# Kernel optimization log

Hardware: AMD Instinct MI355X
Metric: run time of the kernel (lower is better)

## Reference

```python
import jax, jax.numpy as jnp
import numpy as np
import math

B, L, H, E = 16, 1024, 8, 64   # L = nsensor = N (forced by einsum 'bhls,bhlg')
WIN = 1024                      # win_size, last dim of x
G = 64                          # n_group
D_SEL = 1                       # d_sel default


def setup_inputs() -> dict:
    key = jax.random.key(0)
    ks = jax.random.split(key, 7)
    return {
        "queries": jax.random.normal(ks[0], (B, L, H, E), dtype=jnp.float32),
        "keys": jax.random.normal(ks[1], (B, L, H, E), dtype=jnp.float32),
        "values": jax.random.normal(ks[2], (B, L, H, E), dtype=jnp.float32),
        "x": jax.random.normal(ks[3], (B, L, WIN), dtype=jnp.float32),
        "mlp_w": jax.random.normal(ks[4], (H * D_SEL, WIN), dtype=jnp.float32) * 0.02,
        "mlp_b": jax.random.normal(ks[5], (H * D_SEL,), dtype=jnp.float32) * 0.02,
        "sel_W": jax.random.normal(ks[6], (H, G, D_SEL), dtype=jnp.float32),
        "attn_mask": 0,
    }


def _select_attention(x, mlp_w, mlp_b, sel_W, n_heads, d_sel):
    b, n, lwin = x.shape
    xf = x.reshape(b * n, lwin)
    newx = jnp.tanh(xf @ mlp_w.T + mlp_b)                 # [(B*N), H*d_sel]
    # Faithful raw reshape (torch.reshape, no permute): mixes n and h axes.
    newx = newx.reshape(b, n_heads, n, d_sel)             # [B, H, N, d_sel]
    sel = jnp.einsum('bhnd,hgd->bhng', newx, sel_W)       # [B, H, N, G]
    return jax.nn.relu(sel)


def reference(queries, keys, values, x, mlp_w, mlp_b, sel_W, attn_mask):
    b, l, h, e = queries.shape
    scale = 1.0 / math.sqrt(e)
    scores = jnp.einsum('blhe,bshe->bhls', queries, keys)      # [B, H, L, S]
    sel = _select_attention(x, mlp_w, mlp_b, sel_W, h, D_SEL)  # [B, H, L, G]
    scores = jnp.einsum('bhls,bhlg->bhsg', scores, sel)        # [B, H, S, G]
    series = jax.nn.softmax(scale * scores, axis=-1)           # softmax over groups
    # values labeled 'blhs': l=S (value len), s=D (feature). Output V: [B, D, H, G]
    V = jnp.einsum('blhs,bhlg->bshg', values, series)
    return V
```

## Files before the change

kernel.cpp:

```cpp
#include <hip/hip_runtime.h>
#include <math.h>

#define NB 16
#define NL 1024
#define NH 8
#define NE 64
#define NWIN 1024
#define NG 64

#define SCH 128
#define SROW 136

typedef __attribute__((ext_vector_type(8))) short short8;
typedef __attribute__((ext_vector_type(4))) float floatx4;

__device__ __forceinline__ short f2bf(float x) {
    unsigned u = __float_as_uint(x);
    u += 0x7fffu + ((u >> 16) & 1u);
    return (short)(u >> 16);
}
__device__ __forceinline__ float dot4(float4 a, float4 b) {
    return fmaf(a.x, b.x, fmaf(a.y, b.y, fmaf(a.z, b.z, a.w * b.w)));
}

__device__ __forceinline__ void lgkm_barrier() {
    asm volatile("s_waitcnt lgkmcnt(0)" ::: "memory");
    __builtin_amdgcn_s_barrier();
}

__global__ __launch_bounds__(256, 4) void k_sel_q(
    const float* __restrict__ x, const float* __restrict__ mlp_w,
    const float* __restrict__ mlp_b, const float* __restrict__ q,
    float* __restrict__ qp, float* __restrict__ qn)
{
    __shared__ float4 w_lds[8][NWIN / 4];
    __shared__ float t_lds[128];
    __shared__ float redp[4][64], redn[4][64];

    int tid = threadIdx.x;
    int blk = blockIdx.x;
    int ee = blk & 7, bh = blk >> 3;
    int b = bh >> 3, h = bh & 7;
    int w = tid >> 6, lane = tid & 63;
    int sq = lane >> 4, c = lane & 15;

    const float4* w4 = (const float4*)mlp_w;
    float4* wl = (float4*)w_lds;
    #pragma unroll
    for (int i = 0; i < 8; ++i)
        wl[tid + 256 * i] = w4[tid + 256 * i];
    __syncthreads();

    int row_loc = w * 4 + sq;
    int r = b * 1024 + h * 128 + ee * 16 + row_loc;
    const float4* xr = (const float4*)(x + (size_t)r * NWIN);
    float4 a03 = make_float4(0,0,0,0), a47 = make_float4(0,0,0,0);
    #pragma unroll
    for (int i = 0; i < 16; ++i) {
        float4 xv = xr[i * 16 + c];
        a03.x += dot4(xv, w_lds[0][i * 16 + c]);
        a03.y += dot4(xv, w_lds[1][i * 16 + c]);
        a03.z += dot4(xv, w_lds[2][i * 16 + c]);
        a03.w += dot4(xv, w_lds[3][i * 16 + c]);
        a47.x += dot4(xv, w_lds[4][i * 16 + c]);
        a47.y += dot4(xv, w_lds[5][i * 16 + c]);
        a47.z += dot4(xv, w_lds[6][i * 16 + c]);
        a47.w += dot4(xv, w_lds[7][i * 16 + c]);
    }
    #pragma unroll
    for (int off = 1; off < 16; off <<= 1) {
        a03.x += __shfl_xor(a03.x, off, 64);
        a03.y += __shfl_xor(a03.y, off, 64);
        a03.z += __shfl_xor(a03.z, off, 64);
        a03.w += __shfl_xor(a03.w, off, 64);
        a47.x += __shfl_xor(a47.x, off, 64);
        a47.y += __shfl_xor(a47.y, off, 64);
        a47.z += __shfl_xor(a47.z, off, 64);
        a47.w += __shfl_xor(a47.w, off, 64);
    }
    if (c == 0) {
        float4 b03 = *(const float4*)mlp_b;
        float4 b47 = *(const float4*)(mlp_b + 4);
        float4 t03, t47;
        t03.x = tanhf(a03.x + b03.x); t03.y = tanhf(a03.y + b03.y);
        t03.z = tanhf(a03.z + b03.z); t03.w = tanhf(a03.w + b03.w);
        t47.x = tanhf(a47.x + b47.x); t47.y = tanhf(a47.y + b47.y);
        t47.z = tanhf(a47.z + b47.z); t47.w = tanhf(a47.w + b47.w);
        *(float4*)&t_lds[row_loc * 8]     = t03;
        *(float4*)&t_lds[row_loc * 8 + 4] = t47;
    }
    __syncthreads();

    int lo = sq, e4 = c;
    float4 accp = make_float4(0,0,0,0), accn = make_float4(0,0,0,0);
    #pragma unroll
    for (int i = 0; i < 8; ++i) {
        int l_loc = w * 32 + i * 4 + lo;
        float tv = t_lds[l_loc];
        int l = ee * 128 + l_loc;
        float4 qv = *(const float4*)(q + (((size_t)(b * NL + l)) * NH + h) * NE + e4 * 4);
        float tp = fmaxf(tv, 0.f), tn = fminf(tv, 0.f);
        accp.x = fmaf(tp, qv.x, accp.x); accp.y = fmaf(tp, qv.y, accp.y);
        accp.z = fmaf(tp, qv.z, accp.z); accp.w = fmaf(tp, qv.w, accp.w);
        accn.x = fmaf(tn, qv.x, accn.x); accn.y = fmaf(tn, qv.y, accn.y);
        accn.z = fmaf(tn, qv.z, accn.z); accn.w = fmaf(tn, qv.w, accn.w);
    }
    #pragma unroll
    for (int off = 16; off <= 32; off <<= 1) {
        accp.x += __shfl_xor(accp.x, off, 64); accp.y += __shfl_xor(accp.y, off, 64);
        accp.z += __shfl_xor(accp.z, off, 64); accp.w += __shfl_xor(accp.w, off, 64);
        accn.x += __shfl_xor(accn.x, off, 64); accn.y += __shfl_xor(accn.y, off, 64);
        accn.z += __shfl_xor(accn.z, off, 64); accn.w += __shfl_xor(accn.w, off, 64);
    }
    if (lo == 0) {
        *(float4*)&redp[w][e4 * 4] = accp;
        *(float4*)&redn[w][e4 * 4] = accn;
    }
    __syncthreads();
    if (tid < 64) {
        atomicAdd(&qp[bh * NE + tid], redp[0][tid] + redp[1][tid] + redp[2][tid] + redp[3][tid]);
    } else if (tid < 128) {
        int e = tid - 64;
        atomicAdd(&qn[bh * NE + e], redn[0][e] + redn[1][e] + redn[2][e] + redn[3][e]);
    }
}

__global__ __launch_bounds__(256, 4) void k_attn_out(
    const float* __restrict__ keys, const float* __restrict__ values,
    const float* __restrict__ sel_W,
    const float* __restrict__ qp, const float* __restrict__ qn,
    float* __restrict__ out)
{
    __shared__ short sb[NG][SROW];
    __shared__ float ap_l[SCH], an_l[SCH];
    __shared__ float2 wpn[NG];
    __shared__ float mx2[2][SCH], dn2[2][SCH];

    int tid = threadIdx.x, blk = blockIdx.x;
    int chunk = blk & 7, bh = blk >> 3;
    int b = bh >> 3, h = bh & 7;
    int w = tid >> 6, lane = tid & 63;
    int c = lane & 15, sq = lane >> 4;
    const float scale = 0.125f;
    int s0 = chunk * SCH;

    const float4 qp4 = *(const float4*)(qp + bh * NE + c * 4);
    const float4 qn4 = *(const float4*)(qn + bh * NE + c * 4);
    if (tid < NG) {
        float W = sel_W[h * NG + tid];
        wpn[tid] = make_float2(fmaxf(W, 0.f) * scale, fminf(W, 0.f) * scale);
    }

    float4 kvv[8];
    #pragma unroll
    for (int p = 0; p < 8; ++p) {
        int sl = w * 32 + p * 4 + sq;
        kvv[p] = *(const float4*)(keys + (((size_t)(b * NL + s0 + sl)) * NH + h) * NE + c * 4);
    }

    const float* vbase = values + (((size_t)(b * NL + s0)) * NH + h) * NE + 16 * w + c;
    float vregA[16];
    #pragma unroll
    for (int m = 0; m < 16; ++m)
        vregA[m] = vbase[(size_t)((m >> 3) * 32 + sq * 8 + (m & 7)) * (NH * NE)];
    __builtin_amdgcn_sched_barrier(0);

    #pragma unroll
    for (int p = 0; p < 8; ++p) {
        int sl = w * 32 + p * 4 + sq;
        float pp = dot4(kvv[p], qp4);
        float pn = dot4(kvv[p], qn4);
        #pragma unroll
        for (int m_ = 1; m_ <= 8; m_ <<= 1) {
            pp += __shfl_xor(pp, m_, 64);
            pn += __shfl_xor(pn, m_, 64);
        }
        if (c == 0) { ap_l[sl] = pp; an_l[sl] = pn; }
    }

    float vregB[16];
    #pragma unroll
    for (int m = 0; m < 16; ++m)
        vregB[m] = vbase[(size_t)((2 + (m >> 3)) * 32 + sq * 8 + (m & 7)) * (NH * NE)];
    __builtin_amdgcn_sched_barrier(0);

    lgkm_barrier();

    {
        int s_ = tid & 127, gh = tid >> 7, g0 = gh * 32;
        float ap = ap_l[s_], an = an_l[s_];
        float m = -1e30f;
        #pragma unroll 8
        for (int g = 0; g < 32; ++g) {
            float2 wv = wpn[g0 + g];
            m = fmaxf(m, fmaf(wv.x, ap, wv.y * an));
        }
        mx2[gh][s_] = m;
        lgkm_barrier();
        m = fmaxf(mx2[0][s_], mx2[1][s_]);
        float d = 0.f;
        #pragma unroll 8
        for (int g = 0; g < 32; ++g) {
            float2 wv = wpn[g0 + g];
            d += __expf(fmaf(wv.x, ap, wv.y * an) - m);
        }
        dn2[gh][s_] = d;
        lgkm_barrier();
        float inv = 1.0f / (dn2[0][s_] + dn2[1][s_]);
        #pragma unroll 8
        for (int g = 0; g < 32; ++g) {
            float2 wv = wpn[g0 + g];
            sb[g0 + g][s_] = f2bf(__expf(fmaf(wv.x, ap, wv.y * an) - m) * inv);
        }
    }
    lgkm_barrier();

    floatx4 acc[4] = {{0.f,0.f,0.f,0.f},{0.f,0.f,0.f,0.f},
                      {0.f,0.f,0.f,0.f},{0.f,0.f,0.f,0.f}};
    #pragma unroll
    for (int ks = 0; ks < 4; ++ks) {
        short8 av;
        #pragma unroll
        for (int j = 0; j < 8; ++j)
            av[j] = f2bf(ks < 2 ? vregA[ks * 8 + j] : vregB[(ks - 2) * 8 + j]);
        #pragma unroll
        for (int n = 0; n < 4; ++n) {
            short8 bv = *(const short8*)&sb[16 * n + c][ks * 32 + sq * 8];
            acc[n] = __builtin_amdgcn_mfma_f32_16x16x32_bf16(av, bv, acc[n], 0, 0, 0);
        }
    }

    #pragma unroll
    for (int n = 0; n < 4; ++n) {
        #pragma unroll
        for (int r = 0; r < 4; ++r) {
            int e = 16 * w + sq * 4 + r;
            int g = 16 * n + c;
            atomicAdd(&out[((size_t)(b * NE + e) * NH + h) * NG + g], acc[n][r]);
        }
    }
}

extern "C" void kernel_launch(void* const* d_in, const int* in_sizes, int n_in,
                              void* d_out, int out_size, void* d_ws, size_t ws_size,
                              hipStream_t stream) {
    (void)in_sizes; (void)n_in; (void)ws_size;
    const float* queries = (const float*)d_in[0];
    const float* keys    = (const float*)d_in[1];
    const float* values  = (const float*)d_in[2];
    const float* x       = (const float*)d_in[3];
    const float* mlp_w   = (const float*)d_in[4];
    const float* mlp_b   = (const float*)d_in[5];
    const float* sel_W   = (const float*)d_in[6];
    float* out = (float*)d_out;

    float* qp_ws = (float*)d_ws;
    float* qn_ws = qp_ws + NB * NH * NE;

    hipMemsetAsync(out, 0, (size_t)out_size * sizeof(float), stream);
    hipMemsetAsync(qp_ws, 0, (size_t)2 * NB * NH * NE * sizeof(float), stream);

    k_sel_q<<<dim3(NB * NH * 8), dim3(256), 0, stream>>>(x, mlp_w, mlp_b,
                                                          queries, qp_ws, qn_ws);
    k_attn_out<<<dim3(NB * NH * 8), dim3(256), 0, stream>>>(keys, values, sel_W,
                                                            qp_ws, qn_ws, out);
}
```

Baseline: 198.9 us.

## Fuse selection and attention kernels with per-head atomic counter spin-wait

Merges the two kernels into one launch. Each block publishes its partial qp/qn reduction through atomics and a release counter, prefetches keys and values, then spins until all 8 blocks of its (b,h) group have arrived before reading the reduced vectors. Shared memory is aliased between phases. This removes the second launch and the gap between kernels and overlaps K/V loads with the wait. It relies on all blocks being co-resident, which the grid of 1024 blocks at 4 per CU appears to satisfy; otherwise it could deadlock.

```diff
diff --git a/kernel.cpp b/kernel.cpp
--- a/kernel.cpp
+++ b/kernel.cpp
@@ -22,148 +22,169 @@
 __device__ __forceinline__ float dot4(float4 a, float4 b) {
     return fmaf(a.x, b.x, fmaf(a.y, b.y, fmaf(a.z, b.z, a.w * b.w)));
 }
-
 __device__ __forceinline__ void lgkm_barrier() {
     asm volatile("s_waitcnt lgkmcnt(0)" ::: "memory");
     __builtin_amdgcn_s_barrier();
 }
 
-__global__ __launch_bounds__(256, 4) void k_sel_q(
+__global__ __launch_bounds__(256, 4) void k_fused(
     const float* __restrict__ x, const float* __restrict__ mlp_w,
     const float* __restrict__ mlp_b, const float* __restrict__ q,
-    float* __restrict__ qp, float* __restrict__ qn)
+    const float* __restrict__ keys, const float* __restrict__ values,
+    const float* __restrict__ sel_W,
+    float* __restrict__ qp, float* __restrict__ qn,
+    int* __restrict__ cnt, float* __restrict__ out)
 {
-    __shared__ float4 w_lds[8][NWIN / 4];
-    __shared__ float t_lds[128];
-    __shared__ float redp[4][64], redn[4][64];
-
-    int tid = threadIdx.x;
-    int blk = blockIdx.x;
+    __shared__ __align__(16) char smem[35328];
+    float4 (*w_lds)[NWIN / 4] = (float4(*)[NWIN / 4])smem;
+    float*  t_lds             = (float*)(smem + 32768);
+    float  (*redp)[64]        = (float(*)[64])(smem + 33280);
+    float  (*redn)[64]        = (float(*)[64])(smem + 34304);
+    short  (*sb)[SROW]        = (short(*)[SROW])smem;
+    float*  ap_l              = (float*)(smem + 17408);
+    float*  an_l              = (float*)(smem + 17920);
+    float2* wpn               = (float2*)(smem + 18432);
+    float  (*mx2)[SCH]        = (float(*)[SCH])(smem + 18944);
+    float  (*dn2)[SCH]        = (float(*)[SCH])(smem + 19968);
+    float*  qp_l              = (float*)(smem + 20992);
+    float*  qn_l              = (float*)(smem + 21248);
+
+    int tid = threadIdx.x, blk = blockIdx.x;
     int ee = blk & 7, bh = blk >> 3;
     int b = bh >> 3, h = bh & 7;
     int w = tid >> 6, lane = tid & 63;
     int sq = lane >> 4, c = lane & 15;
-
-    const float4* w4 = (const float4*)mlp_w;
-    float4* wl = (float4*)w_lds;
-    #pragma unroll
-    for (int i = 0; i < 8; ++i)
-        wl[tid + 256 * i] = w4[tid + 256 * i];
+    const float scale = 0.125f;
+    int s0 = ee * SCH;
+
+    {
+        const float4* w4 = (const float4*)mlp_w;
+        float4* wl = (float4*)smem;
+        #pragma unroll
+        for (int i = 0; i < 8; ++i)
+            wl[tid + 256 * i] = w4[tid + 256 * i];
+    }
     __syncthreads();
 
-    int row_loc = w * 4 + sq;
-    int r = b * 1024 + h * 128 + ee * 16 + row_loc;
-    const float4* xr = (const float4*)(x + (size_t)r * NWIN);
-    float4 a03 = make_float4(0,0,0,0), a47 = make_float4(0,0,0,0);
-    #pragma unroll
-    for (int i = 0; i < 16; ++i) {
-        float4 xv = xr[i * 16 + c];
-        a03.x += dot4(xv, w_lds[0][i * 16 + c]);
-        a03.y += dot4(xv, w_lds[1][i * 16 + c]);
-        a03.z += dot4(xv, w_lds[2][i * 16 + c]);
-        a03.w += dot4(xv, w_lds[3][i * 16 + c]);
-        a47.x += dot4(xv, w_lds[4][i * 16 + c]);
-        a47.y += dot4(xv, w_lds[5][i * 16 + c]);
-        a47.z += dot4(xv, w_lds[6][i * 16 + c]);
-        a47.w += dot4(xv, w_lds[7][i * 16 + c]);
-    }
-    #pragma unroll
-    for (int off = 1; off < 16; off <<= 1) {
-        a03.x += __shfl_xor(a03.x, off, 64);
-        a03.y += __shfl_xor(a03.y, off, 64);
-        a03.z += __shfl_xor(a03.z, off, 64);
-        a03.w += __shfl_xor(a03.w, off, 64);
-        a47.x += __shfl_xor(a47.x, off, 64);
-        a47.y += __shfl_xor(a47.y, off, 64);
-        a47.z += __shfl_xor(a47.z, off, 64);
-        a47.w += __shfl_xor(a47.w, off, 64);
-    }
-    if (c == 0) {
-        float4 b03 = *(const float4*)mlp_b;
-        float4 b47 = *(const float4*)(mlp_b + 4);
-        float4 t03, t47;
-        t03.x = tanhf(a03.x + b03.x); t03.y = tanhf(a03.y + b03.y);
-        t03.z = tanhf(a03.z + b03.z); t03.w = tanhf(a03.w + b03.w);
-        t47.x = tanhf(a47.x + b47.x); t47.y = tanhf(a47.y + b47.y);
-        t47.z = tanhf(a47.z + b47.z); t47.w = tanhf(a47.w + b47.w);
-        *(float4*)&t_lds[row_loc * 8]     = t03;
-        *(float4*)&t_lds[row_loc * 8 + 4] = t47;
-    }
-    __syncthreads();
-
-    int lo = sq, e4 = c;
-    float4 accp = make_float4(0,0,0,0), accn = make_float4(0,0,0,0);
-    #pragma unroll
-    for (int i = 0; i < 8; ++i) {
-        int l_loc = w * 32 + i * 4 + lo;
-        float tv = t_lds[l_loc];
-        int l = ee * 128 + l_loc;
-        float4 qv = *(const float4*)(q + (((size_t)(b * NL + l)) * NH + h) * NE + e4 * 4);
-        float tp = fmaxf(tv, 0.f), tn = fminf(tv, 0.f);
-        accp.x = fmaf(tp, qv.x, accp.x); accp.y = fmaf(tp, qv.y, accp.y);
-        accp.z = fmaf(tp, qv.z, accp.z); accp.w = fmaf(tp, qv.w, accp.w);
-        accn.x = fmaf(tn, qv.x, accn.x); accn.y = fmaf(tn, qv.y, accn.y);
-        accn.z = fmaf(tn, qv.z, accn.z); accn.w = fmaf(tn, qv.w, accn.w);
-    }
-    #pragma unroll
-    for (int off = 16; off <= 32; off <<= 1) {
-        accp.x += __shfl_xor(accp.x, off, 64); accp.y += __shfl_xor(accp.y, off, 64);
-        accp.z += __shfl_xor(accp.z, off, 64); accp.w += __shfl_xor(accp.w, off, 64);
-        accn.x += __shfl_xor(accn.x, off, 64); accn.y += __shfl_xor(accn.y, off, 64);
-        accn.z += __shfl_xor(accn.z, off, 64); accn.w += __shfl_xor(accn.w, off, 64);
-    }
-    if (lo == 0) {
-        *(float4*)&redp[w][e4 * 4] = accp;
-        *(float4*)&redn[w][e4 * 4] = accn;
-    }
-    __syncthreads();
+    {
+        int row_loc = w * 4 + sq;
+        int r = b * 1024 + h * 128 + ee * 16 + row_loc;
+        const float4* xr = (const float4*)(x + (size_t)r * NWIN);
+        float4 a03 = make_float4(0,0,0,0), a47 = make_float4(0,0,0,0);
+        #pragma unroll
+        for (int i = 0; i < 16; ++i) {
+            float4 xv = xr[i * 16 + c];
+            a03.x += dot4(xv, w_lds[0][i * 16 + c]);
+            a03.y += dot4(xv, w_lds[1][i * 16 + c]);
+            a03.z += dot4(xv, w_lds[2][i * 16 + c]);
+            a03.w += dot4(xv, w_lds[3][i * 16 + c]);
+            a47.x += dot4(xv, w_lds[4][i * 16 + c]);
+            a47.y += dot4(xv, w_lds[5][i * 16 + c]);
+            a47.z += dot4(xv, w_lds[6][i * 16 + c]);
+            a47.w += dot4(xv, w_lds[7][i * 16 + c]);
+        }
+        #pragma unroll
+        for (int off = 1; off < 16; off <<= 1) {
+            a03.x += __shfl_xor(a03.x, off, 64);
+            a03.y += __shfl_xor(a03.y, off, 64);
+            a03.z += __shfl_xor(a03.z, off, 64);
+            a03.w += __shfl_xor(a03.w, off, 64);
+            a47.x += __shfl_xor(a47.x, off, 64);
+            a47.y += __shfl_xor(a47.y, off, 64);
+            a47.z += __shfl_xor(a47.z, off, 64);
+            a47.w += __shfl_xor(a47.w, off, 64);
+        }
+        if (c == 0) {
+            float4 b03 = *(const float4*)mlp_b;
+            float4 b47 = *(const float4*)(mlp_b + 4);
+            float4 t03, t47;
+            t03.x = tanhf(a03.x + b03.x); t03.y = tanhf(a03.y + b03.y);
+            t03.z = tanhf(a03.z + b03.z); t03.w = tanhf(a03.w + b03.w);
+            t47.x = tanhf(a47.x + b47.x); t47.y = tanhf(a47.y + b47.y);
+            t47.z = tanhf(a47.z + b47.z); t47.w = tanhf(a47.w + b47.w);
+            *(float4*)&t_lds[row_loc * 8]     = t03;
+            *(float4*)&t_lds[row_loc * 8 + 4] = t47;
+        }
+    }
+    lgkm_barrier();
+
+    if (tid < NG) {
+        float W = sel_W[h * NG + tid];
+        wpn[tid] = make_float2(fmaxf(W, 0.f) * scale, fminf(W, 0.f) * scale);
+    }
+
+    float4 kvv[8];
+    #pragma unroll
+    for (int p = 0; p < 8; ++p) {
+        int sl = w * 32 + p * 4 + sq;
+        kvv[p] = *(const float4*)(keys + (((size_t)(b * NL + s0 + sl)) * NH + h) * NE + c * 4);
+    }
+
+    {
+        int lo = sq, e4 = c;
+        float4 accp = make_float4(0,0,0,0), accn = make_float4(0,0,0,0);
+        #pragma unroll
+        for (int i = 0; i < 8; ++i) {
+            int l_loc = w * 32 + i * 4 + lo;
+            float tv = t_lds[l_loc];
+            int l = ee * 128 + l_loc;
+            float4 qv = *(const float4*)(q + (((size_t)(b * NL + l)) * NH + h) * NE + e4 * 4);
+            float tp = fmaxf(tv, 0.f), tn = fminf(tv, 0.f);
+            accp.x = fmaf(tp, qv.x, accp.x); accp.y = fmaf(tp, qv.y, accp.y);
+            accp.z = fmaf(tp, qv.z, accp.z); accp.w = fmaf(tp, qv.w, accp.w);
+            accn.x = fmaf(tn, qv.x, accn.x); accn.y = fmaf(tn, qv.y, accn.y);
+            accn.z = fmaf(tn, qv.z, accn.z); accn.w = fmaf(tn, qv.w, accn.w);
+        }
+        #pragma unroll
+        for (int off = 16; off <= 32; off <<= 1) {
+            accp.x += __shfl_xor(accp.x, off, 64); accp.y += __shfl_xor(accp.y, off, 64);
+            accp.z += __shfl_xor(accp.z, off, 64); accp.w += __shfl_xor(accp.w, off, 64);
+            accn.x += __shfl_xor(accn.x, off, 64); accn.y += __shfl_xor(accn.y, off, 64);
+            accn.z += __shfl_xor(accn.z, off, 64); accn.w += __shfl_xor(accn.w, off, 64);
+        }
+        if (lo == 0) {
+            *(float4*)&redp[w][e4 * 4] = accp;
+            *(float4*)&redn[w][e4 * 4] = accn;
+        }
+    }
+    lgkm_barrier();
+
     if (tid < 64) {
         atomicAdd(&qp[bh * NE + tid], redp[0][tid] + redp[1][tid] + redp[2][tid] + redp[3][tid]);
     } else if (tid < 128) {
         int e = tid - 64;
         atomicAdd(&qn[bh * NE + e], redn[0][e] + redn[1][e] + redn[2][e] + redn[3][e]);
     }
-}
-
-__global__ __launch_bounds__(256, 4) void k_attn_out(
-    const float* __restrict__ keys, const float* __restrict__ values,
-    const float* __restrict__ sel_W,
-    const float* __restrict__ qp, const float* __restrict__ qn,
-    float* __restrict__ out)
-{
-    __shared__ short sb[NG][SROW];
-    __shared__ float ap_l[SCH], an_l[SCH];
-    __shared__ float2 wpn[NG];
-    __shared__ float mx2[2][SCH], dn2[2][SCH];
-
-    int tid = threadIdx.x, blk = blockIdx.x;
-    int chunk = blk & 7, bh = blk >> 3;
-    int b = bh >> 3, h = bh & 7;
-    int w = tid >> 6, lane = tid & 63;
-    int c = lane & 15, sq = lane >> 4;
-    const float scale = 0.125f;
-    int s0 = chunk * SCH;
-
-    const float4 qp4 = *(const float4*)(qp + bh * NE + c * 4);
-    const float4 qn4 = *(const float4*)(qn + bh * NE + c * 4);
-    if (tid < NG) {
-        float W = sel_W[h * NG + tid];
-        wpn[tid] = make_float2(fmaxf(W, 0.f) * scale, fminf(W, 0.f) * scale);
-    }
-
-    float4 kvv[8];
-    #pragma unroll
-    for (int p = 0; p < 8; ++p) {
-        int sl = w * 32 + p * 4 + sq;
-        kvv[p] = *(const float4*)(keys + (((size_t)(b * NL + s0 + sl)) * NH + h) * NE + c * 4);
-    }
+    if (tid < 128) __threadfence();
+    __builtin_amdgcn_s_barrier();
+    if (tid == 0)
+        __hip_atomic_fetch_add(&cnt[bh], 1, __ATOMIC_RELEASE, __HIP_MEMORY_SCOPE_AGENT);
 
     const float* vbase = values + (((size_t)(b * NL + s0)) * NH + h) * NE + 16 * w + c;
-    float vregA[16];
+    float vregA[16], vregB[16];
     #pragma unroll
     for (int m = 0; m < 16; ++m)
         vregA[m] = vbase[(size_t)((m >> 3) * 32 + sq * 8 + (m & 7)) * (NH * NE)];
+    #pragma unroll
+    for (int m = 0; m < 16; ++m)
+        vregB[m] = vbase[(size_t)((2 + (m >> 3)) * 32 + sq * 8 + (m & 7)) * (NH * NE)];
     __builtin_amdgcn_sched_barrier(0);
+
+    if (tid == 0) {
+        while (__hip_atomic_load(&cnt[bh], __ATOMIC_ACQUIRE, __HIP_MEMORY_SCOPE_AGENT) < 8)
+            __builtin_amdgcn_s_sleep(2);
+    }
+    __builtin_amdgcn_s_barrier();
+
+    if (tid < 64) {
+        qp_l[tid] = __hip_atomic_load(&qp[bh * NE + tid], __ATOMIC_RELAXED, __HIP_MEMORY_SCOPE_AGENT);
+    } else if (tid < 128) {
+        qn_l[tid - 64] = __hip_atomic_load(&qn[bh * NE + (tid - 64)], __ATOMIC_RELAXED, __HIP_MEMORY_SCOPE_AGENT);
+    }
+    lgkm_barrier();
+
+    const float4 qp4 = *(const float4*)&qp_l[c * 4];
+    const float4 qn4 = *(const float4*)&qn_l[c * 4];
 
     #pragma unroll
     for (int p = 0; p < 8; ++p) {
@@ -177,13 +198,6 @@
         }
         if (c == 0) { ap_l[sl] = pp; an_l[sl] = pn; }
     }
-
-    float vregB[16];
-    #pragma unroll
-    for (int m = 0; m < 16; ++m)
-        vregB[m] = vbase[(size_t)((2 + (m >> 3)) * 32 + sq * 8 + (m & 7)) * (NH * NE)];
-    __builtin_amdgcn_sched_barrier(0);
-
     lgkm_barrier();
 
     {
@@ -233,10 +247,10 @@
     #pragma unroll
     for (int n = 0; n < 4; ++n) {
         #pragma unroll
-        for (int r = 0; r < 4; ++r) {
-            int e = 16 * w + sq * 4 + r;
+        for (int r_ = 0; r_ < 4; ++r_) {
+            int e = 16 * w + sq * 4 + r_;
             int g = 16 * n + c;
-            atomicAdd(&out[((size_t)(b * NE + e) * NH + h) * NG + g], acc[n][r]);
+            atomicAdd(&out[((size_t)(b * NE + e) * NH + h) * NG + g], acc[n][r_]);
         }
     }
 }
@@ -256,12 +270,13 @@
 
     float* qp_ws = (float*)d_ws;
     float* qn_ws = qp_ws + NB * NH * NE;
+    int*   cnt   = (int*)(qn_ws + NB * NH * NE);
 
     hipMemsetAsync(out, 0, (size_t)out_size * sizeof(float), stream);
-    hipMemsetAsync(qp_ws, 0, (size_t)2 * NB * NH * NE * sizeof(float), stream);
-
-    k_sel_q<<<dim3(NB * NH * 8), dim3(256), 0, stream>>>(x, mlp_w, mlp_b,
-                                                          queries, qp_ws, qn_ws);
-    k_attn_out<<<dim3(NB * NH * 8), dim3(256), 0, stream>>>(keys, values, sel_W,
-                                                            qp_ws, qn_ws, out);
-}
+    hipMemsetAsync(qp_ws, 0,
+                   (size_t)2 * NB * NH * NE * sizeof(float) + NB * NH * sizeof(int),
+                   stream);
+
+    k_fused<<<dim3(NB * NH * 8), dim3(256), 0, stream>>>(
+        x, mlp_w, mlp_b, queries, keys, values, sel_W, qp_ws, qn_ws, cnt, out);
+}
```

Measured after the change: 352.5 us. 77.2% more time.

## Make softmax wave-local and replace block barriers with LDS waits

Applied to the files above, without the earlier changes.

Each wave now keeps its own copy of the scaled sel_W weights and computes the softmax for its own 32 sequence rows. The max and denominator partials are combined with a cross-half-wave shuffle instead of shared arrays and block barriers. The second value-register prefetch is moved up alongside the first. In k_sel_q the __syncthreads after the tanh store becomes a plain lgkmcnt wait, which is only safe if every wave reads only t_lds entries written by lanes of the same wave. The aim is to remove several workgroup-wide barriers, at the cost of more LDS for the weight copies and higher register pressure from the earlier loads.

```diff
diff --git a/kernel.cpp b/kernel.cpp
--- a/kernel.cpp
+++ b/kernel.cpp
@@ -22,10 +22,12 @@
 __device__ __forceinline__ float dot4(float4 a, float4 b) {
     return fmaf(a.x, b.x, fmaf(a.y, b.y, fmaf(a.z, b.z, a.w * b.w)));
 }
-
 __device__ __forceinline__ void lgkm_barrier() {
     asm volatile("s_waitcnt lgkmcnt(0)" ::: "memory");
     __builtin_amdgcn_s_barrier();
+}
+__device__ __forceinline__ void lgkm_wait() {
+    asm volatile("s_waitcnt lgkmcnt(0)" ::: "memory");
 }
 
 __global__ __launch_bounds__(256, 4) void k_sel_q(
@@ -89,7 +91,7 @@
         *(float4*)&t_lds[row_loc * 8]     = t03;
         *(float4*)&t_lds[row_loc * 8 + 4] = t47;
     }
-    __syncthreads();
+    lgkm_wait();
 
     int lo = sq, e4 = c;
     float4 accp = make_float4(0,0,0,0), accn = make_float4(0,0,0,0);
@@ -133,8 +135,7 @@
 {
     __shared__ short sb[NG][SROW];
     __shared__ float ap_l[SCH], an_l[SCH];
-    __shared__ float2 wpn[NG];
-    __shared__ float mx2[2][SCH], dn2[2][SCH];
+    __shared__ float2 wpn[4][NG];
 
     int tid = threadIdx.x, blk = blockIdx.x;
     int chunk = blk & 7, bh = blk >> 3;
@@ -144,12 +145,13 @@
     const float scale = 0.125f;
     int s0 = chunk * SCH;
 
+    {
+        float W = sel_W[h * NG + lane];
+        wpn[w][lane] = make_float2(fmaxf(W, 0.f) * scale, fminf(W, 0.f) * scale);
+    }
+
     const float4 qp4 = *(const float4*)(qp + bh * NE + c * 4);
     const float4 qn4 = *(const float4*)(qn + bh * NE + c * 4);
-    if (tid < NG) {
-        float W = sel_W[h * NG + tid];
-        wpn[tid] = make_float2(fmaxf(W, 0.f) * scale, fminf(W, 0.f) * scale);
-    }
 
     float4 kvv[8];
     #pragma unroll
@@ -157,12 +159,14 @@
         int sl = w * 32 + p * 4 + sq;
         kvv[p] = *(const float4*)(keys + (((size_t)(b * NL + s0 + sl)) * NH + h) * NE + c * 4);
     }
-
     const float* vbase = values + (((size_t)(b * NL + s0)) * NH + h) * NE + 16 * w + c;
-    float vregA[16];
+    float vregA[16], vregB[16];
     #pragma unroll
     for (int m = 0; m < 16; ++m)
         vregA[m] = vbase[(size_t)((m >> 3) * 32 + sq * 8 + (m & 7)) * (NH * NE)];
+    #pragma unroll
+    for (int m = 0; m < 16; ++m)
+        vregB[m] = vbase[(size_t)((2 + (m >> 3)) * 32 + sq * 8 + (m & 7)) * (NH * NE)];
     __builtin_amdgcn_sched_barrier(0);
 
     #pragma unroll
@@ -177,39 +181,31 @@
         }
         if (c == 0) { ap_l[sl] = pp; an_l[sl] = pn; }
     }
-
-    float vregB[16];
-    #pragma unroll
-    for (int m = 0; m < 16; ++m)
-        vregB[m] = vbase[(size_t)((2 + (m >> 3)) * 32 + sq * 8 + (m & 7)) * (NH * NE)];
-    __builtin_amdgcn_sched_barrier(0);
-
-    lgkm_barrier();
+    lgkm_wait();
 
     {
-        int s_ = tid & 127, gh = tid >> 7, g0 = gh * 32;
+        int s_ = w * 32 + (lane & 31);
+        int g0 = (lane >> 5) * 32;
         float ap = ap_l[s_], an = an_l[s_];
+        const float2* wv_ = &wpn[w][g0];
         float m = -1e30f;
         #pragma unroll 8
         for (int g = 0; g < 32; ++g) {
-            float2 wv = wpn[g0 + g];
+            float2 wv = wv_[g];
             m = fmaxf(m, fmaf(wv.x, ap, wv.y * an));
         }
-        mx2[gh][s_] = m;
-        lgkm_barrier();
-        m = fmaxf(mx2[0][s_], mx2[1][s_]);
+        m = fmaxf(m, __shfl_xor(m, 32, 64));
         float d = 0.f;
         #pragma unroll 8
         for (int g = 0; g < 32; ++g) {
-            float2 wv = wpn[g0 + g];
+            float2 wv = wv_[g];
             d += __expf(fmaf(wv.x, ap, wv.y * an) - m);
         }
-        dn2[gh][s_] = d;
-        lgkm_barrier();
-        float inv = 1.0f / (dn2[0][s_] + dn2[1][s_]);
+        d += __shfl_xor(d, 32, 64);
+        float inv = 1.0f / d;
         #pragma unroll 8
         for (int g = 0; g < 32; ++g) {
-            float2 wv = wpn[g0 + g];
+            float2 wv = wv_[g];
             sb[g0 + g][s_] = f2bf(__expf(fmaf(wv.x, ap, wv.y * an) - m) * inv);
         }
     }
```

Measured after the change: 199.6 us. No clear change (+0.4%).
